# Kernel tuning notes

Hardware: AMD Instinct MI355X
Metric: run time of the kernel (lower is better)

Reference implementation:

```python
import jax, jax.numpy as jnp
import numpy as np

MAX_WEIGHT = 10.0  # config.max_weight
EPS = 1e-8

BATCH = 2048
VOCAB = 256
SEQ_LEN = 64
NUM_DENDRITES = SEQ_LEN * VOCAB  # 16384


def setup_inputs() -> dict:
    key = jax.random.key(0)
    k1, k2 = jax.random.split(key)
    # binary dendrite activations in {0,1}, stored as float32 as in the torch module
    binary = jax.random.randint(k1, (BATCH, NUM_DENDRITES), 0, 2).astype(jnp.float32)
    # raw_weights ~ Uniform(-1, 1) per nn.init.uniform_
    raw_weights = jax.random.uniform(k2, (VOCAB, NUM_DENDRITES), dtype=jnp.float32,
                                     minval=-1.0, maxval=1.0)
    return {"binary": binary, "raw_weights": raw_weights}


def reference(binary, raw_weights):
    # bounded positive weights: max_weight * sigmoid(raw)
    w = MAX_WEIGHT * jax.nn.sigmoid(raw_weights)            # (vocab, D)
    log_w = jnp.log(jnp.clip(w, EPS))                       # (vocab, D)
    # masked log-sum: where binary==0 the torch code uses log(1)=0, then multiplies
    # by binary anyway, so it is exactly binary @ log_w.T
    log_sum = jnp.einsum('bd,vd->bv', binary, log_w)        # (batch, vocab)
    n_active = jnp.clip(jnp.sum(binary, axis=-1, keepdims=True), 1.0)  # (batch, 1)
    logits = jnp.exp(log_sum / n_active)                    # geometric mean of fired weights
    return logits
```

## Files before the change

### kernel.cpp

```cpp
#include <hip/hip_runtime.h>

#define BATCH 2048
#define VOCAB 256
#define KDIM 16384
#define BM 128
#define BK 32
#define KCHUNK 512
#define NT (KCHUNK / BK)
#define NKCH (KDIM / KCHUNK)
#define LN10 2.302585092994046f

typedef __attribute__((ext_vector_type(8))) short short8;
typedef __attribute__((ext_vector_type(4))) float f32x4;

#define FENCE asm volatile("" ::: "memory")

__device__ __forceinline__ unsigned short f2bf_rne(float f) {
  unsigned int u = __float_as_uint(f);
  u += 0x7fffu + ((u >> 16) & 1u);
  return (unsigned short)(u >> 16);
}
__device__ __forceinline__ unsigned int pack2(float lo, float hi) {
  return (__float_as_uint(lo) >> 16) | (__float_as_uint(hi) & 0xffff0000u);
}

__device__ __forceinline__ void async16(void* lds, const void* g) {
  __builtin_amdgcn_global_load_lds(
      (const __attribute__((address_space(1))) unsigned int*)g,
      (__attribute__((address_space(3))) unsigned int*)lds, 16, 0, 0);
}

__global__ __launch_bounds__(256) void k_logw(const float* __restrict__ raw,
                                              unsigned short* __restrict__ logw) {
  int i = blockIdx.x * 256 + threadIdx.x;
  float4 x = ((const float4*)raw)[i];
  ushort4 r;
  r.x = f2bf_rne(LN10 - log1pf(expf(-x.x)));
  r.y = f2bf_rne(LN10 - log1pf(expf(-x.y)));
  r.z = f2bf_rne(LN10 - log1pf(expf(-x.z)));
  r.w = f2bf_rne(LN10 - log1pf(expf(-x.w)));
  ((ushort4*)logw)[i] = r;
}

__global__ __launch_bounds__(256) void k_gemm(
    const float* __restrict__ binary, const unsigned short* __restrict__ logw,
    float* __restrict__ accb, float* __restrict__ nact) {
  __shared__ char Bsm0[16384];
  __shared__ char Bsm1[16384];

  const int tid = threadIdx.x;
  const int wv = tid >> 6;
  const int lane = tid & 63;
  const int l15 = lane & 15;
  const int lhi = lane >> 4;
  const int m0 = blockIdx.x * BM;
  const int k0 = blockIdx.y * KCHUNK;

  const int brow = lane >> 2;
  const int bks = (lane & 3) ^ ((lane >> 3) & 3);
  const unsigned short* bsrc =
      logw + (size_t)(wv * 64 + brow) * KDIM + k0 + bks * 8;

  const float* asrc0 = binary + (size_t)(m0 + wv * 32 + l15) * KDIM + k0 + lhi * 8;
  const float* asrc1 = asrc0 + (size_t)16 * KDIM;

  const int rdoff = l15 * 64 + ((lhi ^ ((l15 >> 1) & 3)) << 4);

  f32x4 acc[2][16];
#pragma unroll
  for (int m = 0; m < 2; ++m)
#pragma unroll
    for (int n = 0; n < 16; ++n) acc[m][n] = f32x4{0.f, 0.f, 0.f, 0.f};
  float s0 = 0.f, s1 = 0.f;
  float4 Ae[4], Ao[4];

  auto B_STAGE = [&](int t, char* B) {
#pragma unroll
    for (int i = 0; i < 4; ++i)
      async16(B + (wv * 4 + i) * 1024, bsrc + (size_t)i * 16 * KDIM + t * BK);
  };
  auto A_LOAD = [&](int t, float4* A) {
    const float4* p0 = (const float4*)(asrc0 + t * BK);
    const float4* p1 = (const float4*)(asrc1 + t * BK);
    A[0] = p0[0]; A[1] = p0[1]; A[2] = p1[0]; A[3] = p1[1];
  };
  auto COMPUTE = [&](const float4* A, const char* B) {
    s0 += A[0].x + A[0].y + A[0].z + A[0].w + A[1].x + A[1].y + A[1].z + A[1].w;
    s1 += A[2].x + A[2].y + A[2].z + A[2].w + A[3].x + A[3].y + A[3].z + A[3].w;
    union { short8 s; unsigned int u[4]; } a0, a1;
    a0.u[0] = pack2(A[0].x, A[0].y); a0.u[1] = pack2(A[0].z, A[0].w);
    a0.u[2] = pack2(A[1].x, A[1].y); a0.u[3] = pack2(A[1].z, A[1].w);
    a1.u[0] = pack2(A[2].x, A[2].y); a1.u[1] = pack2(A[2].z, A[2].w);
    a1.u[2] = pack2(A[3].x, A[3].y); a1.u[3] = pack2(A[3].z, A[3].w);
#pragma unroll
    for (int n = 0; n < 16; ++n) {
      short8 b = *(const short8*)(B + n * 1024 + rdoff);
      acc[0][n] = __builtin_amdgcn_mfma_f32_16x16x32_bf16(a0.s, b, acc[0][n], 0, 0, 0);
      acc[1][n] = __builtin_amdgcn_mfma_f32_16x16x32_bf16(a1.s, b, acc[1][n], 0, 0, 0);
    }
  };

  B_STAGE(0, Bsm0);
  FENCE;
  A_LOAD(0, Ae);
  FENCE;

#pragma unroll 1
  for (int t = 0; t < NT; t += 2) {
    FENCE;
    __builtin_amdgcn_s_barrier();
    FENCE;
    B_STAGE(t + 1, Bsm1);
    FENCE;
    A_LOAD(t + 1, Ao);
    FENCE;
    asm volatile("s_waitcnt vmcnt(8)" ::: "memory");
    __builtin_amdgcn_s_barrier();
    FENCE;
    COMPUTE(Ae, Bsm0);
    FENCE;
    __builtin_amdgcn_s_barrier();
    FENCE;
    if (t + 2 < NT) {
      B_STAGE(t + 2, Bsm0);
      FENCE;
      A_LOAD(t + 2, Ae);
      FENCE;
      asm volatile("s_waitcnt vmcnt(8)" ::: "memory");
    } else {
      asm volatile("s_waitcnt vmcnt(0)" ::: "memory");
    }
    __builtin_amdgcn_s_barrier();
    FENCE;
    COMPUTE(Ao, Bsm1);
  }

  float t0 = s0, t1 = s1;
  t0 += __shfl_xor(t0, 16, 64); t0 += __shfl_xor(t0, 32, 64);
  t1 += __shfl_xor(t1, 16, 64); t1 += __shfl_xor(t1, 32, 64);
  if (lane < 16) {
    atomicAdd(&nact[m0 + wv * 32 + l15], t0);
    atomicAdd(&nact[m0 + wv * 32 + 16 + l15], t1);
  }

#pragma unroll
  for (int m = 0; m < 2; ++m)
#pragma unroll
    for (int n = 0; n < 16; ++n)
#pragma unroll
      for (int i = 0; i < 4; ++i) {
        int r = m0 + wv * 32 + m * 16 + lhi * 4 + i;
        int c = n * 16 + l15;
        atomicAdd(&accb[(size_t)r * VOCAB + c], acc[m][n][i]);
      }
}

__global__ __launch_bounds__(256) void k_out(float* __restrict__ io,
                                             const float* __restrict__ nact) {
  int b = blockIdx.x;
  int v = threadIdx.x;
  float n = fmaxf(nact[b], 1.0f);
  size_t idx = (size_t)b * VOCAB + v;
  io[idx] = expf(io[idx] / n);
}

extern "C" void kernel_launch(void* const* d_in, const int* in_sizes, int n_in,
                              void* d_out, int out_size, void* d_ws, size_t ws_size,
                              hipStream_t stream) {
  const float* binary = (const float*)d_in[0];
  const float* raw = (const float*)d_in[1];
  float* out = (float*)d_out;
  char* ws = (char*)d_ws;
  unsigned short* logw = (unsigned short*)ws;
  float* nact = (float*)(ws + (size_t)8 * 1024 * 1024);

  hipMemsetAsync(out, 0, (size_t)BATCH * VOCAB * sizeof(float), stream);
  hipMemsetAsync(nact, 0, BATCH * sizeof(float), stream);

  k_logw<<<(VOCAB * KDIM / 4) / 256, 256, 0, stream>>>(raw, logw);

  dim3 g(BATCH / BM, NKCH);
  k_gemm<<<g, 256, 0, stream>>>(binary, logw, out, nact);

  k_out<<<BATCH, VOCAB, 0, stream>>>(out, nact);
}
```

Before: 272.5 us.

## Use 4-stage LDS pipeline, smaller M tile, split-K partials with a reduce kernel

Halves the M tile to 64 rows and cuts split-K from 32 chunks to 8, giving 32x8 blocks with longer K loops. The B/A loads now go through a 4-deep LDS ring buffer with a per-block rotated K start to spread memory traffic. Partial sums are written non-atomically to a workspace and combined by a separate reduce kernel that also applies the exp, which removes the memsets and the float atomics. The cost is a 64KB LDS footprint that limits occupancy, plus extra partial-buffer traffic of about 16MB.

```diff
diff --git a/kernel.cpp b/kernel.cpp
--- a/kernel.cpp
+++ b/kernel.cpp
@@ -3,11 +3,11 @@
 #define BATCH 2048
 #define VOCAB 256
 #define KDIM 16384
-#define BM 128
+#define BM 64
 #define BK 32
-#define KCHUNK 512
+#define S_SPLIT 8
+#define KCHUNK (KDIM / S_SPLIT)
 #define NT (KCHUNK / BK)
-#define NKCH (KDIM / KCHUNK)
 #define LN10 2.302585092994046f
 
 typedef __attribute__((ext_vector_type(8))) short short8;
@@ -42,117 +42,127 @@
   ((ushort4*)logw)[i] = r;
 }
 
+template <int PART>
 __global__ __launch_bounds__(256) void k_gemm(
     const float* __restrict__ binary, const unsigned short* __restrict__ logw,
-    float* __restrict__ accb, float* __restrict__ nact) {
-  __shared__ char Bsm0[16384];
-  __shared__ char Bsm1[16384];
+    float* __restrict__ outp, float* __restrict__ nactp) {
+  __shared__ char smem[65536];
+  char* const Bb0 = smem;
+  char* const Bb1 = smem + 16384;
+  char* const Bb2 = smem + 32768;
+  char* const Bb3 = smem + 49152;
 
   const int tid = threadIdx.x;
   const int wv = tid >> 6;
   const int lane = tid & 63;
   const int l15 = lane & 15;
   const int lhi = lane >> 4;
-  const int m0 = blockIdx.x * BM;
-  const int k0 = blockIdx.y * KCHUNK;
+  const int bx = blockIdx.x;
+  const int by = blockIdx.y;
+  const int phase = ((bx & 7) + by * 8) & (NT - 1);
+
+  const float* asrc =
+      binary + (size_t)(bx * BM + wv * 16 + l15) * KDIM + by * KCHUNK + lhi * 8;
 
   const int brow = lane >> 2;
-  const int bks = (lane & 3) ^ ((lane >> 3) & 3);
+  const int bslot = (lane & 3) ^ (brow & 3);
   const unsigned short* bsrc =
-      logw + (size_t)(wv * 64 + brow) * KDIM + k0 + bks * 8;
-
-  const float* asrc0 = binary + (size_t)(m0 + wv * 32 + l15) * KDIM + k0 + lhi * 8;
-  const float* asrc1 = asrc0 + (size_t)16 * KDIM;
-
-  const int rdoff = l15 * 64 + ((lhi ^ ((l15 >> 1) & 3)) << 4);
-
-  f32x4 acc[2][16];
-#pragma unroll
-  for (int m = 0; m < 2; ++m)
-#pragma unroll
-    for (int n = 0; n < 16; ++n) acc[m][n] = f32x4{0.f, 0.f, 0.f, 0.f};
-  float s0 = 0.f, s1 = 0.f;
-  float4 Ae[4], Ao[4];
-
-  auto B_STAGE = [&](int t, char* B) {
+      logw + (size_t)(wv * 64 + brow) * KDIM + by * KCHUNK + bslot * 8;
+  const int bdst = wv * 4096 + lane * 16;
+
+  const int rdoff = l15 * 64 + ((lhi ^ (l15 & 3)) << 4);
+
+  f32x4 acc[16];
+#pragma unroll
+  for (int n = 0; n < 16; ++n) acc[n] = f32x4{0.f, 0.f, 0.f, 0.f};
+  float asum = 0.f;
+  float4 A0[2], A1[2], A2[2], A3[2];
+
+  auto STAGE = [&](int t, char* B, float4* A) {
+    const int kk = ((t + phase) & (NT - 1)) * BK;
 #pragma unroll
     for (int i = 0; i < 4; ++i)
-      async16(B + (wv * 4 + i) * 1024, bsrc + (size_t)i * 16 * KDIM + t * BK);
+      async16(B + bdst + i * 1024, bsrc + (size_t)i * 16 * KDIM + kk);
+    const float4* p = (const float4*)(asrc + kk);
+    A[0] = p[0];
+    A[1] = p[1];
   };
-  auto A_LOAD = [&](int t, float4* A) {
-    const float4* p0 = (const float4*)(asrc0 + t * BK);
-    const float4* p1 = (const float4*)(asrc1 + t * BK);
-    A[0] = p0[0]; A[1] = p0[1]; A[2] = p1[0]; A[3] = p1[1];
-  };
-  auto COMPUTE = [&](const float4* A, const char* B) {
-    s0 += A[0].x + A[0].y + A[0].z + A[0].w + A[1].x + A[1].y + A[1].z + A[1].w;
-    s1 += A[2].x + A[2].y + A[2].z + A[2].w + A[3].x + A[3].y + A[3].z + A[3].w;
-    union { short8 s; unsigned int u[4]; } a0, a1;
-    a0.u[0] = pack2(A[0].x, A[0].y); a0.u[1] = pack2(A[0].z, A[0].w);
-    a0.u[2] = pack2(A[1].x, A[1].y); a0.u[3] = pack2(A[1].z, A[1].w);
-    a1.u[0] = pack2(A[2].x, A[2].y); a1.u[1] = pack2(A[2].z, A[2].w);
-    a1.u[2] = pack2(A[3].x, A[3].y); a1.u[3] = pack2(A[3].z, A[3].w);
+  auto COMPUTE = [&](const char* B, const float4* A) {
+    asum += A[0].x + A[0].y + A[0].z + A[0].w +
+            A[1].x + A[1].y + A[1].z + A[1].w;
+    union { short8 s; unsigned int u[4]; } af;
+    af.u[0] = pack2(A[0].x, A[0].y);
+    af.u[1] = pack2(A[0].z, A[0].w);
+    af.u[2] = pack2(A[1].x, A[1].y);
+    af.u[3] = pack2(A[1].z, A[1].w);
 #pragma unroll
     for (int n = 0; n < 16; ++n) {
-      short8 b = *(const short8*)(B + n * 1024 + rdoff);
-      acc[0][n] = __builtin_amdgcn_mfma_f32_16x16x32_bf16(a0.s, b, acc[0][n], 0, 0, 0);
-      acc[1][n] = __builtin_amdgcn_mfma_f32_16x16x32_bf16(a1.s, b, acc[1][n], 0, 0, 0);
+      short8 bf = *(const short8*)(B + n * 1024 + rdoff);
+      acc[n] = __builtin_amdgcn_mfma_f32_16x16x32_bf16(bf, af.s, acc[n], 0, 0, 0);
     }
   };
 
-  B_STAGE(0, Bsm0);
-  FENCE;
-  A_LOAD(0, Ae);
-  FENCE;
+#define BAR __builtin_amdgcn_s_barrier()
+#define VMW(N) asm volatile("s_waitcnt vmcnt(" #N ")" ::: "memory")
+
+  STAGE(0, Bb0, A0); FENCE;
+  STAGE(1, Bb1, A1); FENCE;
+  STAGE(2, Bb2, A2); FENCE;
 
 #pragma unroll 1
-  for (int t = 0; t < NT; t += 2) {
-    FENCE;
-    __builtin_amdgcn_s_barrier();
-    FENCE;
-    B_STAGE(t + 1, Bsm1);
-    FENCE;
-    A_LOAD(t + 1, Ao);
-    FENCE;
-    asm volatile("s_waitcnt vmcnt(8)" ::: "memory");
-    __builtin_amdgcn_s_barrier();
-    FENCE;
-    COMPUTE(Ae, Bsm0);
-    FENCE;
-    __builtin_amdgcn_s_barrier();
-    FENCE;
-    if (t + 2 < NT) {
-      B_STAGE(t + 2, Bsm0);
-      FENCE;
-      A_LOAD(t + 2, Ae);
-      FENCE;
-      asm volatile("s_waitcnt vmcnt(8)" ::: "memory");
-    } else {
-      asm volatile("s_waitcnt vmcnt(0)" ::: "memory");
-    }
-    __builtin_amdgcn_s_barrier();
-    FENCE;
-    COMPUTE(Ao, Bsm1);
-  }
-
-  float t0 = s0, t1 = s1;
-  t0 += __shfl_xor(t0, 16, 64); t0 += __shfl_xor(t0, 32, 64);
-  t1 += __shfl_xor(t1, 16, 64); t1 += __shfl_xor(t1, 32, 64);
-  if (lane < 16) {
-    atomicAdd(&nact[m0 + wv * 32 + l15], t0);
-    atomicAdd(&nact[m0 + wv * 32 + 16 + l15], t1);
-  }
-
-#pragma unroll
-  for (int m = 0; m < 2; ++m)
+  for (int t = 0; t < NT - 4; t += 4) {
+    BAR; FENCE; STAGE(t + 3, Bb3, A3); FENCE; VMW(18); BAR; FENCE;
+    COMPUTE(Bb0, A0); FENCE;
+    BAR; FENCE; STAGE(t + 4, Bb0, A0); FENCE; VMW(18); BAR; FENCE;
+    COMPUTE(Bb1, A1); FENCE;
+    BAR; FENCE; STAGE(t + 5, Bb1, A1); FENCE; VMW(18); BAR; FENCE;
+    COMPUTE(Bb2, A2); FENCE;
+    BAR; FENCE; STAGE(t + 6, Bb2, A2); FENCE; VMW(18); BAR; FENCE;
+    COMPUTE(Bb3, A3); FENCE;
+  }
+  BAR; FENCE; STAGE(NT - 1, Bb3, A3); FENCE; VMW(18); BAR; FENCE;
+  COMPUTE(Bb0, A0); FENCE;
+  BAR; FENCE; VMW(12); BAR; FENCE;
+  COMPUTE(Bb1, A1); FENCE;
+  BAR; FENCE; VMW(6); BAR; FENCE;
+  COMPUTE(Bb2, A2); FENCE;
+  BAR; FENCE; VMW(0); BAR; FENCE;
+  COMPUTE(Bb3, A3); FENCE;
+
+  float s = asum;
+  s += __shfl_xor(s, 16, 64);
+  s += __shfl_xor(s, 32, 64);
+  const int row = bx * BM + wv * 16 + l15;
+
+  if (PART) {
+    if (lane < 16) nactp[by * BATCH + row] = s;
+    float* dst = outp + ((size_t)by * BATCH + row) * VOCAB + lhi * 4;
 #pragma unroll
     for (int n = 0; n < 16; ++n)
-#pragma unroll
-      for (int i = 0; i < 4; ++i) {
-        int r = m0 + wv * 32 + m * 16 + lhi * 4 + i;
-        int c = n * 16 + l15;
-        atomicAdd(&accb[(size_t)r * VOCAB + c], acc[m][n][i]);
-      }
+      *(float4*)(dst + n * 16) =
+          (float4){acc[n][0], acc[n][1], acc[n][2], acc[n][3]};
+  } else {
+    if (lane < 16) atomicAdd(&nactp[row], s);
+#pragma unroll
+    for (int n = 0; n < 16; ++n)
+#pragma unroll
+      for (int i = 0; i < 4; ++i)
+        atomicAdd(&outp[(size_t)row * VOCAB + n * 16 + lhi * 4 + i], acc[n][i]);
+  }
+}
+
+__global__ __launch_bounds__(256) void k_reduce(const float* __restrict__ part,
+                                                const float* __restrict__ nactp,
+                                                float* __restrict__ out) {
+  int b = blockIdx.x;
+  int v = threadIdx.x;
+  float sum = 0.f, n = 0.f;
+#pragma unroll
+  for (int i = 0; i < S_SPLIT; ++i) {
+    sum += part[((size_t)i * BATCH + b) * VOCAB + v];
+    n += nactp[i * BATCH + b];
+  }
+  out[(size_t)b * VOCAB + v] = expf(sum / fmaxf(n, 1.f));
 }
 
 __global__ __launch_bounds__(256) void k_out(float* __restrict__ io,
@@ -171,16 +181,24 @@
   const float* raw = (const float*)d_in[1];
   float* out = (float*)d_out;
   char* ws = (char*)d_ws;
+
+  const size_t LOGW_B = (size_t)VOCAB * KDIM * 2;
+  const size_t NACT_B = (size_t)S_SPLIT * BATCH * 4;
+  const size_t PART_B = (size_t)S_SPLIT * BATCH * VOCAB * 4;
   unsigned short* logw = (unsigned short*)ws;
-  float* nact = (float*)(ws + (size_t)8 * 1024 * 1024);
-
-  hipMemsetAsync(out, 0, (size_t)BATCH * VOCAB * sizeof(float), stream);
-  hipMemsetAsync(nact, 0, BATCH * sizeof(float), stream);
+  float* nactp = (float*)(ws + LOGW_B);
+  float* part = (float*)(ws + LOGW_B + NACT_B);
 
   k_logw<<<(VOCAB * KDIM / 4) / 256, 256, 0, stream>>>(raw, logw);
 
-  dim3 g(BATCH / BM, NKCH);
-  k_gemm<<<g, 256, 0, stream>>>(binary, logw, out, nact);
-
-  k_out<<<BATCH, VOCAB, 0, stream>>>(out, nact);
-}
+  dim3 g(BATCH / BM, S_SPLIT);
+  if (ws_size >= LOGW_B + NACT_B + PART_B) {
+    k_gemm<1><<<g, 256, 0, stream>>>(binary, logw, part, nactp);
+    k_reduce<<<BATCH, VOCAB, 0, stream>>>(part, nactp, out);
+  } else {
+    hipMemsetAsync(out, 0, (size_t)BATCH * VOCAB * sizeof(float), stream);
+    hipMemsetAsync(nactp, 0, BATCH * sizeof(float), stream);
+    k_gemm<0><<<g, 256, 0, stream>>>(binary, logw, out, nactp);
+    k_out<<<BATCH, VOCAB, 0, stream>>>(out, nactp);
+  }
+}
```

Result: faster. 240.3 us (-11.8%).
